# Kernel tuning notes

Measured on AMD Instinct MI355X. Metric: run time of the kernel, lower is better.

The kernel has to match this reference:

```python
import jax, jax.numpy as jnp
import numpy as np

S, B, K = 1024, 16, 1024
QD, KD = 1024, 1024


def setup_inputs() -> dict:
    key = jax.random.key(0)
    k1, k2, k3, k4 = jax.random.split(key, 4)
    queries = jax.random.normal(k1, (S, B, QD), dtype=jnp.float32)
    keys = jax.random.normal(k2, (B, K, KD), dtype=jnp.float32)
    null_mask = jax.random.randint(k3, (B, K), 0, 2).astype(jnp.bool_)
    W_in = jax.random.normal(k4, (KD, QD), dtype=jnp.float32) * 0.02
    return {"queries": queries, "keys": keys, "null_mask": null_mask, "W_in": W_in}


def reference(queries, keys, null_mask, W_in):
    # queries: (S, B, QD); keys: (B, K, KD); null_mask: (B, K); W_in: (KD, QD)
    t_query = jnp.einsum('sbq,dq->sbd', queries, W_in)          # linear_in, no bias
    alpha = jnp.einsum('sbd,bkd->sbk', t_query, keys)           # unscaled bilinear scores
    alpha = jnp.where(null_mask[None, :, :], -jnp.inf, alpha)   # masked_fill_
    att_weight = jax.nn.softmax(alpha, axis=2)                  # (S, B, K)
    attened_keys = jnp.einsum('sbk,bkd->sbd', att_weight, keys) # (S, B, KD)
    return (attened_keys, alpha)
```

## Files before the change

### kernel.cpp

```cpp
#include <hip/hip_runtime.h>
#include <math.h>

#define S_DIM 1024
#define B_DIM 16
#define K_DIM 1024
#define QD_DIM 1024
#define KD_DIM 1024
#define MASK_NEG (-3.0e38f)

using short8v = __attribute__((ext_vector_type(8))) short;
using float4v = __attribute__((ext_vector_type(4))) float;
using uint4v  = __attribute__((ext_vector_type(4))) uint;

#define MFMA(a, b, c) __builtin_amdgcn_mfma_f32_16x16x32_bf16(a, b, c, 0, 0, 0)
#define BAR()   __builtin_amdgcn_s_barrier()
#define SB0()   __builtin_amdgcn_sched_barrier(0)
#define PRIO(x) __builtin_amdgcn_s_setprio(x)
#define VMCNT(N) asm volatile("s_waitcnt vmcnt(" #N ")" ::: "memory")
#define LGKM0()  asm volatile("s_waitcnt lgkmcnt(0)" ::: "memory")


__device__ __forceinline__ void gll16(const void* g, void* l) {
    __builtin_amdgcn_global_load_lds((const __attribute__((address_space(1))) unsigned int*)g,
                                     (__attribute__((address_space(3))) unsigned int*)l,
                                     16, 0, 0);
}

__device__ __forceinline__ void split4(const float4 v, uint2& hi, uint2& lo) {
    uint ax = __float_as_uint(v.x), ay = __float_as_uint(v.y);
    uint az = __float_as_uint(v.z), aw = __float_as_uint(v.w);
    hi.x = __builtin_amdgcn_perm(ay, ax, 0x07060302u);
    hi.y = __builtin_amdgcn_perm(aw, az, 0x07060302u);
    float rx = v.x - __uint_as_float(ax & 0xFFFF0000u);
    float ry = v.y - __uint_as_float(ay & 0xFFFF0000u);
    float rz = v.z - __uint_as_float(az & 0xFFFF0000u);
    float rw = v.w - __uint_as_float(aw & 0xFFFF0000u);
    lo.x = __builtin_amdgcn_perm(__float_as_uint(ry), __float_as_uint(rx), 0x07060302u);
    lo.y = __builtin_amdgcn_perm(__float_as_uint(rw), __float_as_uint(rz), 0x07060302u);
}

__device__ __forceinline__ int twiddle(int l) {
    int b0 = (l ^ (l >> 2) ^ (l >> 4)) & 1;
    int b1 = ((l >> 1) ^ (l >> 3)) & 1;
    int b2 = ((l >> 2) ^ (l >> 4)) & 1;
    return (l & 0x38) | (b2 << 2) | (b1 << 1) | b0;
}
__device__ __forceinline__ int fragoff(int R, int quad) {
    return (((R << 2) | quad) ^ (R & 7)) << 3;
}

struct Ctx {
    int w, quad, l15, wm, wn, srow, scol;
    int offA[4], offB[8];
};

__device__ __forceinline__ Ctx make_ctx(int t) {
    Ctx c;
    const int lane = t & 63;
    c.w = t >> 6; c.quad = lane >> 4; c.l15 = lane & 15;
    c.wm = c.w >> 1; c.wn = c.w & 1;
    const int sl = twiddle(lane);
    c.srow = c.w * 32 + (sl >> 2);
    c.scol = (sl & 3) * 8;
    #pragma unroll
    for (int mt = 0; mt < 4; ++mt) { int R = c.wm * 64 + mt * 16 + c.l15; c.offA[mt] = fragoff(R, c.quad); }
    #pragma unroll
    for (int nt = 0; nt < 8; ++nt) { int R = c.wn * 128 + nt * 16 + c.l15; c.offB[nt] = fragoff(R, c.quad); }
    return c;
}

__device__ __forceinline__ void stage2(const short* __restrict__ plane, int row0, int k0,
                                       short* tile, const Ctx& c) {
    const short* g0 = plane + (size_t)(row0 + c.srow) * 1024 + k0 + c.scol;
    gll16(g0, tile + c.w * 1024);
    gll16(g0 + (size_t)16 * 1024, tile + c.w * 1024 + 512);
}

__device__ __forceinline__ void mfma8x4(const short8v (&a)[4], const short8v (&bb)[8],
                                        float4v (&acc)[4][8]) {
    #pragma unroll
    for (int nt = 0; nt < 8; ++nt)
        #pragma unroll
        for (int mt = 0; mt < 4; ++mt)
            acc[mt][nt] = MFMA(a[mt], bb[nt], acc[mt][nt]);
}

template<bool DS>
__device__ __forceinline__ void step_gg(const short* __restrict__ Ahp, const short* __restrict__ Alp,
                                        const short* __restrict__ Bhp, const short* __restrict__ Blp,
                                        int m0, int n0, int kn,
                                        const short* C0, const short* C1, const short* C2, const short* C3,
                                        short* N0, short* N1, short* N2, short* N3,
                                        const Ctx& c, float4v (&acc)[4][8]) {
    short8v ah[4], bh[8];
    #pragma unroll
    for (int mt = 0; mt < 4; ++mt) ah[mt] = *(const short8v*)(C0 + c.offA[mt]);
    #pragma unroll
    for (int nt = 0; nt < 8; ++nt) bh[nt] = *(const short8v*)(C2 + c.offB[nt]);
    if (DS) { stage2(Ahp, m0, kn, N0, c); stage2(Bhp, n0, kn, N2, c); VMCNT(4); }
    else    { VMCNT(0); }
    SB0(); BAR(); LGKM0(); SB0();
    PRIO(1); mfma8x4(ah, bh, acc); PRIO(0); SB0(); BAR();

    short8v al[4];
    #pragma unroll
    for (int mt = 0; mt < 4; ++mt) al[mt] = *(const short8v*)(C1 + c.offA[mt]);
    if (DS) { stage2(Alp, m0, kn, N1, c); stage2(Blp, n0, kn, N3, c); }
    SB0(); BAR(); LGKM0(); SB0();
    PRIO(1); mfma8x4(al, bh, acc); PRIO(0); SB0(); BAR();

    short8v bl[8];
    #pragma unroll
    for (int nt = 0; nt < 8; ++nt) bl[nt] = *(const short8v*)(C3 + c.offB[nt]);
    if (DS) { VMCNT(4); }
    SB0(); BAR(); LGKM0(); SB0();
    PRIO(1); mfma8x4(ah, bl, acc); PRIO(0); SB0(); BAR();
}

__device__ __forceinline__ void core_gg(const short* __restrict__ Ahp, const short* __restrict__ Alp,
                                        const short* __restrict__ Bhp, const short* __restrict__ Blp,
                                        int m0, int n0, short* lds, const Ctx& c, float4v (&acc)[4][8]) {
    short *T00 = lds,         *T01 = lds + 8192,  *T02 = lds + 16384, *T03 = lds + 24576;
    short *T10 = lds + 32768, *T11 = lds + 40960, *T12 = lds + 49152, *T13 = lds + 57344;
    stage2(Ahp, m0, 0, T00, c); stage2(Bhp, n0, 0, T02, c);
    stage2(Alp, m0, 0, T01, c); stage2(Blp, n0, 0, T03, c);
    VMCNT(4); SB0(); BAR();
    #pragma unroll 1
    for (int it = 0; it < 15; ++it) {
        step_gg<true>(Ahp, Alp, Bhp, Blp, m0, n0, (2 * it + 1) * 32, T00, T01, T02, T03, T10, T11, T12, T13, c, acc);
        step_gg<true>(Ahp, Alp, Bhp, Blp, m0, n0, (2 * it + 2) * 32, T10, T11, T12, T13, T00, T01, T02, T03, c, acc);
    }
    step_gg<true >(Ahp, Alp, Bhp, Blp, m0, n0, 31 * 32, T00, T01, T02, T03, T10, T11, T12, T13, c, acc);
    step_gg<false>(Ahp, Alp, Bhp, Blp, m0, n0, 0,       T10, T11, T12, T13, T00, T01, T02, T03, c, acc);
}

__global__ __launch_bounds__(256) void k_split(const float* __restrict__ src,
                                               short* __restrict__ h, short* __restrict__ l) {
    const size_t base = ((size_t)blockIdx.x * 256 + threadIdx.x) * 4;
    const float4 v = *(const float4*)(src + base);
    uint2 hh, ll;
    split4(v, hh, ll);
    *(uint2*)(h + base) = hh;
    *(uint2*)(l + base) = ll;
}

__global__ __launch_bounds__(256) void k_transpose(const float* __restrict__ keys,
                                                   short* __restrict__ th, short* __restrict__ tl) {
    __shared__ float T[32][33];
    const int t = threadIdx.x;
    const int b = blockIdx.z, d0 = blockIdx.x * 32, k0 = blockIdx.y * 32;
    const float* Kb = keys + (size_t)b * K_DIM * KD_DIM;
    const int ry = t >> 3, cx = (t & 7) * 4;
    const float4 v = *(const float4*)(Kb + (size_t)(k0 + ry) * KD_DIM + d0 + cx);
    T[ry][cx] = v.x; T[ry][cx + 1] = v.y; T[ry][cx + 2] = v.z; T[ry][cx + 3] = v.w;
    __syncthreads();
    float4 g;
    g.x = T[cx][ry]; g.y = T[cx + 1][ry]; g.z = T[cx + 2][ry]; g.w = T[cx + 3][ry];
    uint2 hh, ll;
    split4(g, hh, ll);
    const size_t o = (size_t)b * K_DIM * KD_DIM + (size_t)(d0 + ry) * K_DIM + k0 + cx;
    *(uint2*)(th + o) = hh;
    *(uint2*)(tl + o) = ll;
}

__global__ __launch_bounds__(256) void k_stats(const float* __restrict__ alpha,
                                               float* __restrict__ mx,
                                               float* __restrict__ il) {
    const int r = blockIdx.x;
    const int t = threadIdx.x;
    const float4 v = ((const float4*)(alpha + (size_t)r * K_DIM))[t];
    float m = fmaxf(fmaxf(v.x, v.y), fmaxf(v.z, v.w));
    #pragma unroll
    for (int o = 1; o < 64; o <<= 1) m = fmaxf(m, __shfl_xor(m, o, 64));
    __shared__ float redm[4];
    __shared__ float reds[4];
    const int wid = t >> 6;
    if ((t & 63) == 0) redm[wid] = m;
    __syncthreads();
    const float M = fmaxf(fmaxf(redm[0], redm[1]), fmaxf(redm[2], redm[3]));
    float s = expf(v.x - M) + expf(v.y - M) + expf(v.z - M) + expf(v.w - M);
    #pragma unroll
    for (int o = 1; o < 64; o <<= 1) s += __shfl_xor(s, o, 64);
    if ((t & 63) == 0) reds[wid] = s;
    __syncthreads();
    if (t == 0) {
        mx[r] = M;
        il[r] = 1.0f / (reds[0] + reds[1] + reds[2] + reds[3]);
    }
}

__global__ __launch_bounds__(256) void k_copy(const float4* __restrict__ src, float4* __restrict__ dst) {
    const size_t i = (size_t)blockIdx.x * 256 + threadIdx.x;
    dst[i] = src[i];
}

__global__ __launch_bounds__(512, 2) void g1k(const short* __restrict__ Qh, const short* __restrict__ Ql,
                                              const short* __restrict__ Wh, const short* __restrict__ Wl,
                                              short* __restrict__ TQh, short* __restrict__ TQl) {
    __shared__ __align__(16) short lds[65536];
    const int t = threadIdx.x;
    const int m0 = blockIdx.y * 256, n0 = blockIdx.x * 256;
    const Ctx c = make_ctx(t);
    float4v acc[4][8] = {};
    core_gg(Qh, Ql, Wh, Wl, m0, n0, lds, c, acc);
    #pragma unroll
    for (int mt = 0; mt < 4; ++mt)
        #pragma unroll
        for (int reg = 0; reg < 4; ++reg) {
            const int m = m0 + c.wm * 64 + mt * 16 + c.quad * 4 + reg;
            const int s = m >> 4, bq = m & 15;
            short* th = TQh + (size_t)bq * 1048576 + (size_t)s * 1024;
            short* tl = TQl + (size_t)bq * 1048576 + (size_t)s * 1024;
            #pragma unroll
            for (int nt = 0; nt < 8; ++nt) {
                const int n = n0 + c.wn * 128 + nt * 16 + c.l15;
                const float x = acc[mt][nt][reg];
                const uint u = __float_as_uint(x);
                th[n] = (short)(u >> 16);
                const float r2 = x - __uint_as_float(u & 0xFFFF0000u);
                tl[n] = (short)(__float_as_uint(r2) >> 16);
            }
        }
}

__global__ __launch_bounds__(512, 2) void g2k(const short* __restrict__ TQh, const short* __restrict__ TQl,
                                              const short* __restrict__ Kh, const short* __restrict__ Kl,
                                              const int* __restrict__ mask, float* __restrict__ alpha) {
    __shared__ __align__(16) short lds[65536];
    const int t = threadIdx.x;
    const int m0 = blockIdx.y * 256, n0 = blockIdx.x * 256, b = blockIdx.z;
    const Ctx c = make_ctx(t);
    float4v acc[4][8] = {};
    core_gg(TQh + (size_t)b * 1048576, TQl + (size_t)b * 1048576,
            Kh + (size_t)b * 1048576, Kl + (size_t)b * 1048576, m0, n0, lds, c, acc);
    int mk[8];
    #pragma unroll
    for (int nt = 0; nt < 8; ++nt)
        mk[nt] = mask[b * K_DIM + n0 + c.wn * 128 + nt * 16 + c.l15];
    #pragma unroll
    for (int mt = 0; mt < 4; ++mt)
        #pragma unroll
        for (int reg = 0; reg < 4; ++reg) {
            const int m = m0 + c.wm * 64 + mt * 16 + c.quad * 4 + reg;
            #pragma unroll
            for (int nt = 0; nt < 8; ++nt) {
                const int n = n0 + c.wn * 128 + nt * 16 + c.l15;
                alpha[((size_t)m * B_DIM + b) * K_DIM + n] = mk[nt] ? MASK_NEG : acc[mt][nt][reg];
            }
        }
}

__device__ __forceinline__ void writeA(const float4 (&va)[4], float Mv, float Lv,
                                       short* N0, short* N1, int ws0, int ws1) {
    uint2 h[4], l[4];
    #pragma unroll
    for (int i = 0; i < 4; ++i) {
        float4 p;
        p.x = __expf(va[i].x - Mv) * Lv;
        p.y = __expf(va[i].y - Mv) * Lv;
        p.z = __expf(va[i].z - Mv) * Lv;
        p.w = __expf(va[i].w - Mv) * Lv;
        split4(p, h[i], l[i]);
    }
    uint4v v0, v1;
    v0[0] = h[0].x; v0[1] = h[0].y; v0[2] = h[1].x; v0[3] = h[1].y;
    v1[0] = h[2].x; v1[1] = h[2].y; v1[2] = h[3].x; v1[3] = h[3].y;
    *(uint4v*)(N0 + ws0 * 8) = v0;
    *(uint4v*)(N0 + ws1 * 8) = v1;
    v0[0] = l[0].x; v0[1] = l[0].y; v0[2] = l[1].x; v0[3] = l[1].y;
    v1[0] = l[2].x; v1[1] = l[2].y; v1[2] = l[3].x; v1[3] = l[3].y;
    *(uint4v*)(N1 + ws0 * 8) = v0;
    *(uint4v*)(N1 + ws1 * 8) = v1;
}

template<bool DS>
__device__ __forceinline__ void step_g3(const float4* __restrict__ aP, int kn,
                                        const short* __restrict__ Bhp, const short* __restrict__ Blp, int n0,
                                        const short* C0, const short* C1, const short* C2, const short* C3,
                                        short* N0, short* N1, short* N2, short* N3,
                                        const Ctx& c, float Mv, float Lv, int ws0, int ws1,
                                        float4v (&acc)[4][8]) {
    short8v ah[4], bh[8];
    #pragma unroll
    for (int mt = 0; mt < 4; ++mt) ah[mt] = *(const short8v*)(C0 + c.offA[mt]);
    #pragma unroll
    for (int nt = 0; nt < 8; ++nt) bh[nt] = *(const short8v*)(C2 + c.offB[nt]);
    float4 va[4];
    if (DS) {
        #pragma unroll
        for (int i = 0; i < 4; ++i) va[i] = aP[kn / 4 + i];
        stage2(Bhp, n0, kn, N2, c);
    }
    SB0(); BAR(); LGKM0(); SB0();
    PRIO(1); mfma8x4(ah, bh, acc); PRIO(0); SB0(); BAR();

    short8v al[4];
    #pragma unroll
    for (int mt = 0; mt < 4; ++mt) al[mt] = *(const short8v*)(C1 + c.offA[mt]);
    if (DS) { stage2(Blp, n0, kn, N3, c); }
    SB0(); BAR(); LGKM0(); SB0();
    PRIO(1); mfma8x4(al, bh, acc); PRIO(0); SB0(); BAR();

    if (DS) { VMCNT(4); }
    else    { VMCNT(0); }
    SB0(); BAR();
    short8v bl[8];
    #pragma unroll
    for (int nt = 0; nt < 8; ++nt) bl[nt] = *(const short8v*)(C3 + c.offB[nt]);
    LGKM0(); SB0();
    PRIO(1); mfma8x4(ah, bl, acc); PRIO(0);
    if (DS) {
        writeA(va, Mv, Lv, N0, N1, ws0, ws1);
        LGKM0();
        VMCNT(2);
    }
    SB0(); BAR();
}

__global__ __launch_bounds__(512, 2) void g3k(const float* __restrict__ alpha,
                                              const short* __restrict__ KTh, const short* __restrict__ KTl,
                                              const float* __restrict__ mx, const float* __restrict__ il,
                                              float* __restrict__ outk) {
    __shared__ __align__(16) short lds[65536];
    const int t = threadIdx.x;
    const int m0 = blockIdx.y * 256, n0 = blockIdx.x * 256, b = blockIdx.z;
    const Ctx c = make_ctx(t);
    const short* Bhp = KTh + (size_t)b * 1048576;
    const short* Blp = KTl + (size_t)b * 1048576;
    const int arow = t >> 1, ac = t & 1;
    const float4* aP = (const float4*)(alpha + ((size_t)(m0 + arow) * B_DIM + b) * K_DIM + ac * 16);
    const float Mv = mx[(size_t)(m0 + arow) * B_DIM + b];
    const float Lv = il[(size_t)(m0 + arow) * B_DIM + b];
    const int c0 = ac * 2;
    const int ws0 = ((arow << 2) | c0) ^ (arow & 7);
    const int ws1 = ((arow << 2) | (c0 + 1)) ^ (arow & 7);
    short *T00 = lds,         *T01 = lds + 8192,  *T02 = lds + 16384, *T03 = lds + 24576;
    short *T10 = lds + 32768, *T11 = lds + 40960, *T12 = lds + 49152, *T13 = lds + 57344;

    float4v acc[4][8] = {};
    {
        float4 va[4];
        #pragma unroll
        for (int i = 0; i < 4; ++i) va[i] = aP[i];
        stage2(Bhp, n0, 0, T02, c);
        stage2(Blp, n0, 0, T03, c);
        VMCNT(4);
        writeA(va, Mv, Lv, T00, T01, ws0, ws1);
        LGKM0();
        VMCNT(2);
        SB0(); BAR();
    }
    #pragma unroll 1
    for (int it = 0; it < 15; ++it) {
        step_g3<true>(aP, (2 * it + 1) * 32, Bhp, Blp, n0, T00, T01, T02, T03, T10, T11, T12, T13, c, Mv, Lv, ws0, ws1, acc);
        step_g3<true>(aP, (2 * it + 2) * 32, Bhp, Blp, n0, T10, T11, T12, T13, T00, T01, T02, T03, c, Mv, Lv, ws0, ws1, acc);
    }
    step_g3<true >(aP, 31 * 32, Bhp, Blp, n0, T00, T01, T02, T03, T10, T11, T12, T13, c, Mv, Lv, ws0, ws1, acc);
    step_g3<false>(aP, 0,       Bhp, Blp, n0, T10, T11, T12, T13, T00, T01, T02, T03, c, Mv, Lv, ws0, ws1, acc);

    #pragma unroll
    for (int mt = 0; mt < 4; ++mt)
        #pragma unroll
        for (int reg = 0; reg < 4; ++reg) {
            const int m = m0 + c.wm * 64 + mt * 16 + c.quad * 4 + reg;
            #pragma unroll
            for (int nt = 0; nt < 8; ++nt) {
                const int n = n0 + c.wn * 128 + nt * 16 + c.l15;
                outk[((size_t)m * B_DIM + b) * KD_DIM + n] = acc[mt][nt][reg];
            }
        }
}

extern "C" void kernel_launch(void* const* d_in, const int* in_sizes, int n_in,
                              void* d_out, int out_size, void* d_ws, size_t ws_size,
                              hipStream_t stream) {
    const float* Q    = (const float*)d_in[0];
    const float* keys = (const float*)d_in[1];
    const int*   mask = (const int*)d_in[2];
    const float* W    = (const float*)d_in[3];

    float* out_att   = (float*)d_out;
    float* out_alpha = out_att + (size_t)S_DIM * B_DIM * KD_DIM;

    const size_t PLW    = 1048576;
    const size_t STREAM = (size_t)B_DIM * PLW;

    short *Wh, *Wl, *Qh, *Ql, *Khs, *Kls, *KTh, *KTl, *TQh, *TQl;
    float *mx, *il, *g3out;
    bool small_ws;
    char* ws = (char*)d_ws;

    if (ws_size >= ((size_t)261 << 20)) {
        small_ws = false;
        Wh  = (short*)ws;          Wl  = Wh + PLW;
        Qh  = Wl + PLW;            Ql  = Qh + STREAM;
        Khs = Ql + STREAM;         Kls = Khs + STREAM;
        KTh = Kls + STREAM;        KTl = KTh + STREAM;
        TQh = KTl + STREAM;        TQl = TQh + STREAM;
        mx  = (float*)(TQl + STREAM);
        il  = mx + S_DIM * B_DIM;
        g3out = out_att;
    } else {
        small_ws = true;
        TQh = (short*)ws;          TQl = TQh + STREAM;
        mx  = (float*)((char*)ws + ((size_t)64 << 20));
        il  = mx + S_DIM * B_DIM;
        Wh  = (short*)out_att;     Wl  = Wh + PLW;
        Qh  = (short*)out_alpha;   Ql  = Qh + STREAM;
        Khs = (short*)out_att;     Kls = Khs + STREAM;
        KTh = Khs;                 KTl = Kls;
        g3out = (float*)ws;
    }

    dim3 blk(256);
    dim3 blkg(512);

    k_split<<<dim3(1024), blk, 0, stream>>>(W, Wh, Wl);
    k_split<<<dim3(16384), blk, 0, stream>>>(Q, Qh, Ql);

    g1k<<<dim3(KD_DIM / 256, (S_DIM * B_DIM) / 256), blkg, 0, stream>>>(Qh, Ql, Wh, Wl, TQh, TQl);

    k_split<<<dim3(16384), blk, 0, stream>>>(keys, Khs, Kls);

    g2k<<<dim3(K_DIM / 256, S_DIM / 256, B_DIM), blkg, 0, stream>>>(TQh, TQl, Khs, Kls, mask, out_alpha);

    k_transpose<<<dim3(32, 32, B_DIM), blk, 0, stream>>>(keys, KTh, KTl);

    k_stats<<<dim3(S_DIM * B_DIM), blk, 0, stream>>>(out_alpha, mx, il);

    g3k<<<dim3(KD_DIM / 256, S_DIM / 256, B_DIM), blkg, 0, stream>>>(out_alpha, KTh, KTl, mx, il, g3out);

    if (small_ws)
        k_copy<<<dim3((S_DIM * B_DIM * KD_DIM) / (4 * 256)), blk, 0, stream>>>((const float4*)g3out,
                                                                               (float4*)out_att);
}
```

Before: 556.5 us.

## Fuse fp32-to-bf16 split and transpose into GEMM staging, drop prep kernels

The separate split kernels for Q and keys and the keys transpose kernel are removed. Each GEMM now loads raw fp32 tiles from global memory into registers, splits them into hi/lo bf16 and writes them into swizzled LDS tiles inside its pipelined main loop. This avoids several full-size intermediate round trips through memory and the extra launches, and it also makes the workspace fallback and final copy unnecessary. In exchange, every GEMM block redoes the split work, g3k reads keys with strided, transposing fp32 loads, and waits on vmcnt(0) each step, which weakens the overlap of loads with compute.

```diff
diff --git a/kernel.cpp b/kernel.cpp
--- a/kernel.cpp
+++ b/kernel.cpp
@@ -51,6 +51,7 @@
 
 struct Ctx {
     int w, quad, l15, wm, wn, srow, scol;
+    int arow, ac, ws0, ws1;
     int offA[4], offB[8];
 };
 
@@ -62,6 +63,10 @@
     const int sl = twiddle(lane);
     c.srow = c.w * 32 + (sl >> 2);
     c.scol = (sl & 3) * 8;
+    c.arow = t >> 1; c.ac = t & 1;
+    const int c0 = c.ac * 2;
+    c.ws0 = ((c.arow << 2) | c0) ^ (c.arow & 7);
+    c.ws1 = ((c.arow << 2) | (c0 + 1)) ^ (c.arow & 7);
     #pragma unroll
     for (int mt = 0; mt < 4; ++mt) { int R = c.wm * 64 + mt * 16 + c.l15; c.offA[mt] = fragoff(R, c.quad); }
     #pragma unroll
@@ -85,53 +90,58 @@
             acc[mt][nt] = MFMA(a[mt], bb[nt], acc[mt][nt]);
 }
 
-template<bool DS>
-__device__ __forceinline__ void step_gg(const short* __restrict__ Ahp, const short* __restrict__ Alp,
-                                        const short* __restrict__ Bhp, const short* __restrict__ Blp,
-                                        int m0, int n0, int kn,
-                                        const short* C0, const short* C1, const short* C2, const short* C3,
-                                        short* N0, short* N1, short* N2, short* N3,
-                                        const Ctx& c, float4v (&acc)[4][8]) {
-    short8v ah[4], bh[8];
-    #pragma unroll
-    for (int mt = 0; mt < 4; ++mt) ah[mt] = *(const short8v*)(C0 + c.offA[mt]);
-    #pragma unroll
-    for (int nt = 0; nt < 8; ++nt) bh[nt] = *(const short8v*)(C2 + c.offB[nt]);
-    if (DS) { stage2(Ahp, m0, kn, N0, c); stage2(Bhp, n0, kn, N2, c); VMCNT(4); }
-    else    { VMCNT(0); }
-    SB0(); BAR(); LGKM0(); SB0();
-    PRIO(1); mfma8x4(ah, bh, acc); PRIO(0); SB0(); BAR();
-
-    short8v al[4];
-    #pragma unroll
-    for (int mt = 0; mt < 4; ++mt) al[mt] = *(const short8v*)(C1 + c.offA[mt]);
-    if (DS) { stage2(Alp, m0, kn, N1, c); stage2(Blp, n0, kn, N3, c); }
-    SB0(); BAR(); LGKM0(); SB0();
-    PRIO(1); mfma8x4(al, bh, acc); PRIO(0); SB0(); BAR();
-
-    short8v bl[8];
-    #pragma unroll
-    for (int nt = 0; nt < 8; ++nt) bl[nt] = *(const short8v*)(C3 + c.offB[nt]);
-    if (DS) { VMCNT(4); }
-    SB0(); BAR(); LGKM0(); SB0();
-    PRIO(1); mfma8x4(ah, bl, acc); PRIO(0); SB0(); BAR();
-}
-
-__device__ __forceinline__ void core_gg(const short* __restrict__ Ahp, const short* __restrict__ Alp,
-                                        const short* __restrict__ Bhp, const short* __restrict__ Blp,
-                                        int m0, int n0, short* lds, const Ctx& c, float4v (&acc)[4][8]) {
-    short *T00 = lds,         *T01 = lds + 8192,  *T02 = lds + 16384, *T03 = lds + 24576;
-    short *T10 = lds + 32768, *T11 = lds + 40960, *T12 = lds + 49152, *T13 = lds + 57344;
-    stage2(Ahp, m0, 0, T00, c); stage2(Bhp, n0, 0, T02, c);
-    stage2(Alp, m0, 0, T01, c); stage2(Blp, n0, 0, T03, c);
-    VMCNT(4); SB0(); BAR();
-    #pragma unroll 1
-    for (int it = 0; it < 15; ++it) {
-        step_gg<true>(Ahp, Alp, Bhp, Blp, m0, n0, (2 * it + 1) * 32, T00, T01, T02, T03, T10, T11, T12, T13, c, acc);
-        step_gg<true>(Ahp, Alp, Bhp, Blp, m0, n0, (2 * it + 2) * 32, T10, T11, T12, T13, T00, T01, T02, T03, c, acc);
-    }
-    step_gg<true >(Ahp, Alp, Bhp, Blp, m0, n0, 31 * 32, T00, T01, T02, T03, T10, T11, T12, T13, c, acc);
-    step_gg<false>(Ahp, Alp, Bhp, Blp, m0, n0, 0,       T10, T11, T12, T13, T00, T01, T02, T03, c, acc);
+__device__ __forceinline__ void load4(const float4* __restrict__ P, int kn, float4 (&v)[4]) {
+    #pragma unroll
+    for (int i = 0; i < 4; ++i) v[i] = P[kn / 4 + i];
+}
+
+__device__ __forceinline__ void write_split(const float4 (&va)[4], short* N0, short* N1,
+                                            int ws0, int ws1) {
+    uint2 h[4], l[4];
+    #pragma unroll
+    for (int i = 0; i < 4; ++i) split4(va[i], h[i], l[i]);
+    uint4v v0, v1;
+    v0[0] = h[0].x; v0[1] = h[0].y; v0[2] = h[1].x; v0[3] = h[1].y;
+    v1[0] = h[2].x; v1[1] = h[2].y; v1[2] = h[3].x; v1[3] = h[3].y;
+    *(uint4v*)(N0 + ws0 * 8) = v0;
+    *(uint4v*)(N0 + ws1 * 8) = v1;
+    v0[0] = l[0].x; v0[1] = l[0].y; v0[2] = l[1].x; v0[3] = l[1].y;
+    v1[0] = l[2].x; v1[1] = l[2].y; v1[2] = l[3].x; v1[3] = l[3].y;
+    *(uint4v*)(N1 + ws0 * 8) = v0;
+    *(uint4v*)(N1 + ws1 * 8) = v1;
+}
+
+__device__ __forceinline__ void writeA_exp(const float4 (&va)[4], float Mv, float Lv,
+                                           short* N0, short* N1, int ws0, int ws1) {
+    float4 p[4];
+    #pragma unroll
+    for (int i = 0; i < 4; ++i) {
+        p[i].x = __expf(va[i].x - Mv) * Lv;
+        p[i].y = __expf(va[i].y - Mv) * Lv;
+        p[i].z = __expf(va[i].z - Mv) * Lv;
+        p[i].w = __expf(va[i].w - Mv) * Lv;
+    }
+    write_split(p, N0, N1, ws0, ws1);
+}
+
+__device__ __forceinline__ void loadT(const float* __restrict__ fB, int kn, float4 (&f)[4]) {
+    #pragma unroll
+    for (int i = 0; i < 4; ++i) f[i] = *(const float4*)(fB + (size_t)(kn + i) * 1024);
+}
+__device__ __forceinline__ void writeT(const float4 (&f)[4], short* N2, short* N3,
+                                       int kq, int dd) {
+    #pragma unroll
+    for (int e = 0; e < 4; ++e) {
+        float4 g;
+        g.x = (&f[0].x)[e]; g.y = (&f[1].x)[e];
+        g.z = (&f[2].x)[e]; g.w = (&f[3].x)[e];
+        uint2 h, l;
+        split4(g, h, l);
+        const int R = dd * 4 + e;
+        const int byteoff = ((((R << 2) | (kq >> 1)) ^ (R & 7)) << 4) + (kq & 1) * 8;
+        *(uint2*)((char*)N2 + byteoff) = h;
+        *(uint2*)((char*)N3 + byteoff) = l;
+    }
 }
 
 __global__ __launch_bounds__(256) void k_split(const float* __restrict__ src,
@@ -144,25 +154,6 @@
     *(uint2*)(l + base) = ll;
 }
 
-__global__ __launch_bounds__(256) void k_transpose(const float* __restrict__ keys,
-                                                   short* __restrict__ th, short* __restrict__ tl) {
-    __shared__ float T[32][33];
-    const int t = threadIdx.x;
-    const int b = blockIdx.z, d0 = blockIdx.x * 32, k0 = blockIdx.y * 32;
-    const float* Kb = keys + (size_t)b * K_DIM * KD_DIM;
-    const int ry = t >> 3, cx = (t & 7) * 4;
-    const float4 v = *(const float4*)(Kb + (size_t)(k0 + ry) * KD_DIM + d0 + cx);
-    T[ry][cx] = v.x; T[ry][cx + 1] = v.y; T[ry][cx + 2] = v.z; T[ry][cx + 3] = v.w;
-    __syncthreads();
-    float4 g;
-    g.x = T[cx][ry]; g.y = T[cx + 1][ry]; g.z = T[cx + 2][ry]; g.w = T[cx + 3][ry];
-    uint2 hh, ll;
-    split4(g, hh, ll);
-    const size_t o = (size_t)b * K_DIM * KD_DIM + (size_t)(d0 + ry) * K_DIM + k0 + cx;
-    *(uint2*)(th + o) = hh;
-    *(uint2*)(tl + o) = ll;
-}
-
 __global__ __launch_bounds__(256) void k_stats(const float* __restrict__ alpha,
                                                float* __restrict__ mx,
                                                float* __restrict__ il) {
@@ -189,20 +180,75 @@
     }
 }
 
-__global__ __launch_bounds__(256) void k_copy(const float4* __restrict__ src, float4* __restrict__ dst) {
-    const size_t i = (size_t)blockIdx.x * 256 + threadIdx.x;
-    dst[i] = src[i];
-}
-
-__global__ __launch_bounds__(512, 2) void g1k(const short* __restrict__ Qh, const short* __restrict__ Ql,
+template<bool DS>
+__device__ __forceinline__ void step_g1(const float4* __restrict__ qP, int kn,
+                                        const short* __restrict__ Wh, const short* __restrict__ Wl, int n0,
+                                        const short* C0, const short* C1, const short* C2, const short* C3,
+                                        short* N0, short* N1, short* N2, short* N3,
+                                        const Ctx& c, float4v (&acc)[4][8]) {
+    short8v ah[4], bh[8];
+    #pragma unroll
+    for (int mt = 0; mt < 4; ++mt) ah[mt] = *(const short8v*)(C0 + c.offA[mt]);
+    #pragma unroll
+    for (int nt = 0; nt < 8; ++nt) bh[nt] = *(const short8v*)(C2 + c.offB[nt]);
+    float4 qv[4];
+    if (DS) { load4(qP, kn, qv); SB0(); stage2(Wh, n0, kn, N2, c); }
+    SB0(); BAR(); LGKM0(); SB0();
+    PRIO(1); mfma8x4(ah, bh, acc); PRIO(0); SB0(); BAR();
+
+    short8v al[4];
+    #pragma unroll
+    for (int mt = 0; mt < 4; ++mt) al[mt] = *(const short8v*)(C1 + c.offA[mt]);
+    if (DS) { stage2(Wl, n0, kn, N3, c); }
+    SB0(); BAR(); LGKM0(); SB0();
+    PRIO(1); mfma8x4(al, bh, acc); PRIO(0); SB0(); BAR();
+
+    if (DS) { VMCNT(4); } else { VMCNT(0); }
+    SB0(); BAR();
+    short8v bl[8];
+    #pragma unroll
+    for (int nt = 0; nt < 8; ++nt) bl[nt] = *(const short8v*)(C3 + c.offB[nt]);
+    LGKM0(); SB0();
+    PRIO(1); mfma8x4(ah, bl, acc); PRIO(0);
+    if (DS) {
+        write_split(qv, N0, N1, c.ws0, c.ws1);
+        LGKM0();
+        VMCNT(2);
+    }
+    SB0(); BAR();
+}
+
+__global__ __launch_bounds__(512, 2) void g1k(const float* __restrict__ Q,
                                               const short* __restrict__ Wh, const short* __restrict__ Wl,
                                               short* __restrict__ TQh, short* __restrict__ TQl) {
     __shared__ __align__(16) short lds[65536];
     const int t = threadIdx.x;
     const int m0 = blockIdx.y * 256, n0 = blockIdx.x * 256;
     const Ctx c = make_ctx(t);
+    const float4* qP = (const float4*)(Q + (size_t)(m0 + c.arow) * QD_DIM + c.ac * 16);
+    short *T00 = lds,         *T01 = lds + 8192,  *T02 = lds + 16384, *T03 = lds + 24576;
+    short *T10 = lds + 32768, *T11 = lds + 40960, *T12 = lds + 49152, *T13 = lds + 57344;
+
     float4v acc[4][8] = {};
-    core_gg(Qh, Ql, Wh, Wl, m0, n0, lds, c, acc);
+    {
+        float4 qv[4];
+        load4(qP, 0, qv); SB0();
+        stage2(Wh, n0, 0, T02, c);
+        stage2(Wl, n0, 0, T03, c);
+        VMCNT(4); SB0();
+        write_split(qv, T00, T01, c.ws0, c.ws1);
+        LGKM0();
+        VMCNT(2); SB0();
+        BAR();
+    }
+    #pragma unroll 1
+    for (int it = 0; it < 15; ++it) {
+        step_g1<true>(qP, (2 * it + 1) * 32, Wh, Wl, n0, T00, T01, T02, T03, T10, T11, T12, T13, c, acc);
+        step_g1<true>(qP, (2 * it + 2) * 32, Wh, Wl, n0, T10, T11, T12, T13, T00, T01, T02, T03, c, acc);
+    }
+    step_g1<true >(qP, 31 * 32, Wh, Wl, n0, T00, T01, T02, T03, T10, T11, T12, T13, c, acc);
+    step_g1<false>(qP, 0,       Wh, Wl, n0, T10, T11, T12, T13, T00, T01, T02, T03, c, acc);
+
     #pragma unroll
     for (int mt = 0; mt < 4; ++mt)
         #pragma unroll
@@ -223,16 +269,79 @@
         }
 }
 
+template<bool DS>
+__device__ __forceinline__ void step_g2(const float4* __restrict__ kP, int kn,
+                                        const short* __restrict__ Ahp, const short* __restrict__ Alp, int m0,
+                                        const short* C0, const short* C1, const short* C2, const short* C3,
+                                        short* N0, short* N1, short* N2, short* N3,
+                                        const Ctx& c, float4v (&acc)[4][8]) {
+    short8v ah[4], bh[8];
+    #pragma unroll
+    for (int mt = 0; mt < 4; ++mt) ah[mt] = *(const short8v*)(C0 + c.offA[mt]);
+    #pragma unroll
+    for (int nt = 0; nt < 8; ++nt) bh[nt] = *(const short8v*)(C2 + c.offB[nt]);
+    float4 kv[4];
+    if (DS) { load4(kP, kn, kv); SB0(); stage2(Ahp, m0, kn, N0, c); VMCNT(6); }
+    else    { VMCNT(0); }
+    SB0(); BAR(); LGKM0(); SB0();
+    PRIO(1); mfma8x4(ah, bh, acc); PRIO(0); SB0(); BAR();
+
+    short8v al[4];
+    #pragma unroll
+    for (int mt = 0; mt < 4; ++mt) al[mt] = *(const short8v*)(C1 + c.offA[mt]);
+    if (DS) { stage2(Alp, m0, kn, N1, c); }
+    SB0(); BAR(); LGKM0(); SB0();
+    PRIO(1); mfma8x4(al, bh, acc); PRIO(0); SB0(); BAR();
+
+    if (DS) { VMCNT(4); } else { VMCNT(0); }
+    SB0(); BAR();
+    short8v bl[8];
+    #pragma unroll
+    for (int nt = 0; nt < 8; ++nt) bl[nt] = *(const short8v*)(C3 + c.offB[nt]);
+    LGKM0(); SB0();
+    PRIO(1); mfma8x4(ah, bl, acc); PRIO(0);
+    if (DS) {
+        write_split(kv, N2, N3, c.ws0, c.ws1);
+        LGKM0();
+        VMCNT(2);
+    }
+    SB0(); BAR();
+}
+
 __global__ __launch_bounds__(512, 2) void g2k(const short* __restrict__ TQh, const short* __restrict__ TQl,
-                                              const short* __restrict__ Kh, const short* __restrict__ Kl,
+                                              const float* __restrict__ keys,
                                               const int* __restrict__ mask, float* __restrict__ alpha) {
     __shared__ __align__(16) short lds[65536];
     const int t = threadIdx.x;
     const int m0 = blockIdx.y * 256, n0 = blockIdx.x * 256, b = blockIdx.z;
     const Ctx c = make_ctx(t);
+    const short* Ahp = TQh + (size_t)b * 1048576;
+    const short* Alp = TQl + (size_t)b * 1048576;
+    const float* Kb = keys + (size_t)b * K_DIM * KD_DIM;
+    const float4* kP = (const float4*)(Kb + (size_t)(n0 + c.arow) * KD_DIM + c.ac * 16);
+    short *T00 = lds,         *T01 = lds + 8192,  *T02 = lds + 16384, *T03 = lds + 24576;
+    short *T10 = lds + 32768, *T11 = lds + 40960, *T12 = lds + 49152, *T13 = lds + 57344;
+
     float4v acc[4][8] = {};
-    core_gg(TQh + (size_t)b * 1048576, TQl + (size_t)b * 1048576,
-            Kh + (size_t)b * 1048576, Kl + (size_t)b * 1048576, m0, n0, lds, c, acc);
+    {
+        float4 kv[4];
+        load4(kP, 0, kv); SB0();
+        stage2(Ahp, m0, 0, T00, c);
+        VMCNT(2); SB0();
+        write_split(kv, T02, T03, c.ws0, c.ws1);
+        LGKM0(); SB0();
+        stage2(Alp, m0, 0, T01, c);
+        VMCNT(2); SB0();
+        BAR();
+    }
+    #pragma unroll 1
+    for (int it = 0; it < 15; ++it) {
+        step_g2<true>(kP, (2 * it + 1) * 32, Ahp, Alp, m0, T00, T01, T02, T03, T10, T11, T12, T13, c, acc);
+        step_g2<true>(kP, (2 * it + 2) * 32, Ahp, Alp, m0, T10, T11, T12, T13, T00, T01, T02, T03, c, acc);
+    }
+    step_g2<true >(kP, 31 * 32, Ahp, Alp, m0, T00, T01, T02, T03, T10, T11, T12, T13, c, acc);
+    step_g2<false>(kP, 0,       Ahp, Alp, m0, T10, T11, T12, T13, T00, T01, T02, T03, c, acc);
+
     int mk[8];
     #pragma unroll
     for (int nt = 0; nt < 8; ++nt)
@@ -250,59 +359,31 @@
         }
 }
 
-__device__ __forceinline__ void writeA(const float4 (&va)[4], float Mv, float Lv,
-                                       short* N0, short* N1, int ws0, int ws1) {
-    uint2 h[4], l[4];
-    #pragma unroll
-    for (int i = 0; i < 4; ++i) {
-        float4 p;
-        p.x = __expf(va[i].x - Mv) * Lv;
-        p.y = __expf(va[i].y - Mv) * Lv;
-        p.z = __expf(va[i].z - Mv) * Lv;
-        p.w = __expf(va[i].w - Mv) * Lv;
-        split4(p, h[i], l[i]);
-    }
-    uint4v v0, v1;
-    v0[0] = h[0].x; v0[1] = h[0].y; v0[2] = h[1].x; v0[3] = h[1].y;
-    v1[0] = h[2].x; v1[1] = h[2].y; v1[2] = h[3].x; v1[3] = h[3].y;
-    *(uint4v*)(N0 + ws0 * 8) = v0;
-    *(uint4v*)(N0 + ws1 * 8) = v1;
-    v0[0] = l[0].x; v0[1] = l[0].y; v0[2] = l[1].x; v0[3] = l[1].y;
-    v1[0] = l[2].x; v1[1] = l[2].y; v1[2] = l[3].x; v1[3] = l[3].y;
-    *(uint4v*)(N1 + ws0 * 8) = v0;
-    *(uint4v*)(N1 + ws1 * 8) = v1;
-}
-
 template<bool DS>
-__device__ __forceinline__ void step_g3(const float4* __restrict__ aP, int kn,
-                                        const short* __restrict__ Bhp, const short* __restrict__ Blp, int n0,
+__device__ __forceinline__ void step_g3(const float4* __restrict__ aP, const float* __restrict__ fB, int kn,
                                         const short* C0, const short* C1, const short* C2, const short* C3,
                                         short* N0, short* N1, short* N2, short* N3,
-                                        const Ctx& c, float Mv, float Lv, int ws0, int ws1,
+                                        const Ctx& c, float Mv, float Lv, int kq, int dd,
                                         float4v (&acc)[4][8]) {
     short8v ah[4], bh[8];
     #pragma unroll
     for (int mt = 0; mt < 4; ++mt) ah[mt] = *(const short8v*)(C0 + c.offA[mt]);
     #pragma unroll
     for (int nt = 0; nt < 8; ++nt) bh[nt] = *(const short8v*)(C2 + c.offB[nt]);
-    float4 va[4];
-    if (DS) {
-        #pragma unroll
-        for (int i = 0; i < 4; ++i) va[i] = aP[kn / 4 + i];
-        stage2(Bhp, n0, kn, N2, c);
-    }
+    float4 av[4];
+    if (DS) { load4(aP, kn, av); }
     SB0(); BAR(); LGKM0(); SB0();
     PRIO(1); mfma8x4(ah, bh, acc); PRIO(0); SB0(); BAR();
 
     short8v al[4];
     #pragma unroll
     for (int mt = 0; mt < 4; ++mt) al[mt] = *(const short8v*)(C1 + c.offA[mt]);
-    if (DS) { stage2(Blp, n0, kn, N3, c); }
+    float4 f[4];
+    if (DS) { loadT(fB, kn, f); }
     SB0(); BAR(); LGKM0(); SB0();
     PRIO(1); mfma8x4(al, bh, acc); PRIO(0); SB0(); BAR();
 
-    if (DS) { VMCNT(4); }
-    else    { VMCNT(0); }
+    VMCNT(0);
     SB0(); BAR();
     short8v bl[8];
     #pragma unroll
@@ -310,53 +391,48 @@
     LGKM0(); SB0();
     PRIO(1); mfma8x4(ah, bl, acc); PRIO(0);
     if (DS) {
-        writeA(va, Mv, Lv, N0, N1, ws0, ws1);
+        writeA_exp(av, Mv, Lv, N0, N1, c.ws0, c.ws1);
+        writeT(f, N2, N3, kq, dd);
         LGKM0();
-        VMCNT(2);
     }
     SB0(); BAR();
 }
 
 __global__ __launch_bounds__(512, 2) void g3k(const float* __restrict__ alpha,
-                                              const short* __restrict__ KTh, const short* __restrict__ KTl,
+                                              const float* __restrict__ keys,
                                               const float* __restrict__ mx, const float* __restrict__ il,
                                               float* __restrict__ outk) {
     __shared__ __align__(16) short lds[65536];
     const int t = threadIdx.x;
     const int m0 = blockIdx.y * 256, n0 = blockIdx.x * 256, b = blockIdx.z;
     const Ctx c = make_ctx(t);
-    const short* Bhp = KTh + (size_t)b * 1048576;
-    const short* Blp = KTl + (size_t)b * 1048576;
-    const int arow = t >> 1, ac = t & 1;
-    const float4* aP = (const float4*)(alpha + ((size_t)(m0 + arow) * B_DIM + b) * K_DIM + ac * 16);
-    const float Mv = mx[(size_t)(m0 + arow) * B_DIM + b];
-    const float Lv = il[(size_t)(m0 + arow) * B_DIM + b];
-    const int c0 = ac * 2;
-    const int ws0 = ((arow << 2) | c0) ^ (arow & 7);
-    const int ws1 = ((arow << 2) | (c0 + 1)) ^ (arow & 7);
+    const float* Kb = keys + (size_t)b * K_DIM * KD_DIM;
+    const float4* aP = (const float4*)(alpha + ((size_t)(m0 + c.arow) * B_DIM + b) * K_DIM + c.ac * 16);
+    const float Mv = mx[(size_t)(m0 + c.arow) * B_DIM + b];
+    const float Lv = il[(size_t)(m0 + c.arow) * B_DIM + b];
+    const int kq = t & 7, dd = t >> 3;
+    const float* fB = Kb + (size_t)(4 * kq) * KD_DIM + n0 + dd * 4;
     short *T00 = lds,         *T01 = lds + 8192,  *T02 = lds + 16384, *T03 = lds + 24576;
     short *T10 = lds + 32768, *T11 = lds + 40960, *T12 = lds + 49152, *T13 = lds + 57344;
 
     float4v acc[4][8] = {};
     {
-        float4 va[4];
-        #pragma unroll
-        for (int i = 0; i < 4; ++i) va[i] = aP[i];
-        stage2(Bhp, n0, 0, T02, c);
-        stage2(Blp, n0, 0, T03, c);
-        VMCNT(4);
-        writeA(va, Mv, Lv, T00, T01, ws0, ws1);
-        LGKM0();
-        VMCNT(2);
-        SB0(); BAR();
+        float4 av[4], f[4];
+        load4(aP, 0, av); SB0();
+        loadT(fB, 0, f);
+        VMCNT(0); SB0();
+        writeA_exp(av, Mv, Lv, T00, T01, c.ws0, c.ws1);
+        writeT(f, T02, T03, kq, dd);
+        LGKM0(); SB0();
+        BAR();
     }
     #pragma unroll 1
     for (int it = 0; it < 15; ++it) {
-        step_g3<true>(aP, (2 * it + 1) * 32, Bhp, Blp, n0, T00, T01, T02, T03, T10, T11, T12, T13, c, Mv, Lv, ws0, ws1, acc);
-        step_g3<true>(aP, (2 * it + 2) * 32, Bhp, Blp, n0, T10, T11, T12, T13, T00, T01, T02, T03, c, Mv, Lv, ws0, ws1, acc);
-    }
-    step_g3<true >(aP, 31 * 32, Bhp, Blp, n0, T00, T01, T02, T03, T10, T11, T12, T13, c, Mv, Lv, ws0, ws1, acc);
-    step_g3<false>(aP, 0,       Bhp, Blp, n0, T10, T11, T12, T13, T00, T01, T02, T03, c, Mv, Lv, ws0, ws1, acc);
+        step_g3<true>(aP, fB, (2 * it + 1) * 32, T00, T01, T02, T03, T10, T11, T12, T13, c, Mv, Lv, kq, dd, acc);
+        step_g3<true>(aP, fB, (2 * it + 2) * 32, T10, T11, T12, T13, T00, T01, T02, T03, c, Mv, Lv, kq, dd, acc);
+    }
+    step_g3<true >(aP, fB, 31 * 32, T00, T01, T02, T03, T10, T11, T12, T13, c, Mv, Lv, kq, dd, acc);
+    step_g3<false>(aP, fB, 0,       T10, T11, T12, T13, T00, T01, T02, T03, c, Mv, Lv, kq, dd, acc);
 
     #pragma unroll
     for (int mt = 0; mt < 4; ++mt)
@@ -382,55 +458,25 @@
     float* out_att   = (float*)d_out;
     float* out_alpha = out_att + (size_t)S_DIM * B_DIM * KD_DIM;
 
-    const size_t PLW    = 1048576;
-    const size_t STREAM = (size_t)B_DIM * PLW;
-
-    short *Wh, *Wl, *Qh, *Ql, *Khs, *Kls, *KTh, *KTl, *TQh, *TQl;
-    float *mx, *il, *g3out;
-    bool small_ws;
-    char* ws = (char*)d_ws;
-
-    if (ws_size >= ((size_t)261 << 20)) {
-        small_ws = false;
-        Wh  = (short*)ws;          Wl  = Wh + PLW;
-        Qh  = Wl + PLW;            Ql  = Qh + STREAM;
-        Khs = Ql + STREAM;         Kls = Khs + STREAM;
-        KTh = Kls + STREAM;        KTl = KTh + STREAM;
-        TQh = KTl + STREAM;        TQl = TQh + STREAM;
-        mx  = (float*)(TQl + STREAM);
-        il  = mx + S_DIM * B_DIM;
-        g3out = out_att;
-    } else {
-        small_ws = true;
-        TQh = (short*)ws;          TQl = TQh + STREAM;
-        mx  = (float*)((char*)ws + ((size_t)64 << 20));
-        il  = mx + S_DIM * B_DIM;
-        Wh  = (short*)out_att;     Wl  = Wh + PLW;
-        Qh  = (short*)out_alpha;   Ql  = Qh + STREAM;
-        Khs = (short*)out_att;     Kls = Khs + STREAM;
-        KTh = Khs;                 KTl = Kls;
-        g3out = (float*)ws;
-    }
-
-    dim3 blk(256);
-    dim3 blkg(512);
+    const size_t STREAM = (size_t)B_DIM * 1048576;
+
+    short* TQh = (short*)d_ws;
+    short* TQl = TQh + STREAM;
+    float* mx  = (float*)((char*)d_ws + ((size_t)64 << 20));
+    float* il  = mx + S_DIM * B_DIM;
+
+    short* Wh = (short*)out_att;
+    short* Wl = Wh + 1048576;
+
+    dim3 blk(256), blkg(512);
 
     k_split<<<dim3(1024), blk, 0, stream>>>(W, Wh, Wl);
-    k_split<<<dim3(16384), blk, 0, stream>>>(Q, Qh, Ql);
-
-    g1k<<<dim3(KD_DIM / 256, (S_DIM * B_DIM) / 256), blkg, 0, stream>>>(Qh, Ql, Wh, Wl, TQh, TQl);
-
-    k_split<<<dim3(16384), blk, 0, stream>>>(keys, Khs, Kls);
-
-    g2k<<<dim3(K_DIM / 256, S_DIM / 256, B_DIM), blkg, 0, stream>>>(TQh, TQl, Khs, Kls, mask, out_alpha);
-
-    k_transpose<<<dim3(32, 32, B_DIM), blk, 0, stream>>>(keys, KTh, KTl);
+
+    g1k<<<dim3(KD_DIM / 256, (S_DIM * B_DIM) / 256), blkg, 0, stream>>>(Q, Wh, Wl, TQh, TQl);
+
+    g2k<<<dim3(K_DIM / 256, S_DIM / 256, B_DIM), blkg, 0, stream>>>(TQh, TQl, keys, mask, out_alpha);
 
     k_stats<<<dim3(S_DIM * B_DIM), blk, 0, stream>>>(out_alpha, mx, il);
 
-    g3k<<<dim3(KD_DIM / 256, S_DIM / 256, B_DIM), blkg, 0, stream>>>(out_alpha, KTh, KTl, mx, il, g3out);
-
-    if (small_ws)
-        k_copy<<<dim3((S_DIM * B_DIM * KD_DIM) / (4 * 256)), blk, 0, stream>>>((const float4*)g3out,
-                                                                               (float4*)out_att);
-}
+    g3k<<<dim3(KD_DIM / 256, S_DIM / 256, B_DIM), blkg, 0, stream>>>(out_alpha, keys, mx, il, out_att);
+}
```

Measured after the change: 596.9 us. 1.07x slower.
